# Kernel tuning notes

Measured on AMD Instinct MI355X. Metric: run time of the kernel, lower is better.

## Reference

```python
import jax, jax.numpy as jnp
import numpy as np

N = 50000        # nodes
E_RAND = 800000  # random edges (avg degree 16)
F_IN = 512       # num_features
H = 128          # h_dim * num_heads = 16 * 8
C = 40           # num_classes
NEG_SLOPE = 0.2  # GATv2 default


def _glorot(key, shape):
    lim = float(np.sqrt(6.0 / (shape[0] + shape[1])))
    return jax.random.uniform(key, shape, jnp.float32, -lim, lim)


def setup_inputs() -> dict:
    key = jax.random.key(0)
    ks = jax.random.split(key, 12)
    src = jax.random.randint(ks[0], (E_RAND,), 0, N)
    dst = jax.random.randint(ks[1], (E_RAND,), 0, N)
    loop = jnp.arange(N)  # self-loops (GATv2Conv add_self_loops=True)
    edge_index = jnp.stack([jnp.concatenate([src, loop]),
                            jnp.concatenate([dst, loop])]).astype(jnp.int32)
    x = jax.random.normal(ks[2], (N, F_IN), jnp.float32)
    return {
        "x": x,
        "edge_index": edge_index,
        "W1l": _glorot(ks[3], (F_IN, H)), "b1l": jnp.zeros((H,), jnp.float32),
        "W1r": _glorot(ks[4], (F_IN, H)), "b1r": jnp.zeros((H,), jnp.float32),
        "a1": _glorot(ks[5], (H, 1)).reshape(H),
        "bias1": jnp.zeros((H,), jnp.float32),
        "W2l": _glorot(ks[6], (H, C)), "b2l": jnp.zeros((C,), jnp.float32),
        "W2r": _glorot(ks[7], (H, C)), "b2r": jnp.zeros((C,), jnp.float32),
        "a2": _glorot(ks[8], (C, 1)).reshape(C),
        "bias2": jnp.zeros((C,), jnp.float32),
    }


def gatv2_layer(x, src, dst, Wl, bl, Wr, br, att, bias, n):
    # PyG GATv2Conv, heads=1: xl = lin_l(x) (source side), xr = lin_r(x) (target side)
    xl = x @ Wl + bl                                   # [N, C_out]
    xr = x @ Wr + br                                   # [N, C_out]
    # edge score e_ij = a^T LeakyReLU(xl[j] + xr[i])
    e = jax.nn.leaky_relu(xl[src] + xr[dst], negative_slope=NEG_SLOPE) @ att  # [E]
    # segment softmax over edges grouped by destination node
    m = jax.ops.segment_max(e, dst, num_segments=n)    # every node has a self-loop
    ex = jnp.exp(e - m[dst])
    den = jax.ops.segment_sum(ex, dst, num_segments=n)
    alpha = ex / den[dst]                              # [E]
    # weighted scatter-aggregate of source-transformed features
    out = jax.ops.segment_sum(alpha[:, None] * xl[src], dst, num_segments=n)
    return out + bias


def reference(x, edge_index, W1l, b1l, W1r, b1r, a1, bias1,
              W2l, b2l, W2r, b2r, a2, bias2):
    # eval mode: dropout(p=0.6) is identity
    src, dst = edge_index[0], edge_index[1]
    n = x.shape[0]
    h = gatv2_layer(x, src, dst, W1l, b1l, W1r, b1r, a1, bias1, n)
    h = jax.nn.elu(h)
    h = gatv2_layer(h, src, dst, W2l, b2l, W2r, b2r, a2, bias2, n)
    return (h, jax.nn.log_softmax(h, axis=1))
```

## Files before the change

### kernel.cpp

```cpp
#include <hip/hip_runtime.h>
#include <hip/hip_bf16.h>
#include <math.h>

#define FIN 512
#define H1 128
#define C2 40
#define C2P 64

typedef __attribute__((ext_vector_type(8))) short short8;
typedef __attribute__((ext_vector_type(4))) float f32x4;

__device__ __forceinline__ ushort f2bf(float f) {
    union { float f; unsigned u; } c; c.f = f;
    unsigned u = c.u;
    return (ushort)((u + 0x7fffu + ((u >> 16) & 1u)) >> 16);
}
__device__ __forceinline__ float bf2f_lo(unsigned u) { return __uint_as_float(u << 16); }
__device__ __forceinline__ float bf2f_hi(unsigned u) { return __uint_as_float(u & 0xffff0000u); }

__device__ __forceinline__ short bfc(float f) {
    __hip_bfloat16 h = __float2bfloat16(f);
    return *reinterpret_cast<short*>(&h);
}

__device__ __forceinline__ void gload_lds16(const void* g, void* l) {
    __builtin_amdgcn_global_load_lds(
        (const __attribute__((address_space(1))) void*)g,
        (__attribute__((address_space(3))) void*)l, 16, 0, 0);
}

__global__ void aux_k(const int* __restrict__ dst, int* __restrict__ cnt, int E, int EB,
                      const float* __restrict__ W1l, const float* __restrict__ W1r,
                      ushort* __restrict__ Wt2,
                      const float* __restrict__ W2l, const float* __restrict__ W2r,
                      ushort* __restrict__ Ws) {
    int b = blockIdx.x;
    int t = threadIdx.x;
    if (b < EB) {
        int e = b * 256 + t;
        if (e < E) atomicAdd(&cnt[dst[e] + 1], 1);
    } else if (b < EB + 512) {
        int idx = (b - EB) * 256 + t;
        int kc  = idx >> 11;
        int rem = idx & 2047;
        int col = rem >> 3;
        int j   = rem & 7;
        int k   = kc * 8 + j;
        float v = (col < H1) ? W1l[k * H1 + col] : W1r[k * H1 + (col - H1)];
        Wt2[idx] = f2bf(v);
    } else {
        int idx = (b - EB - 512) * 256 + t;
        if (idx < 80 * H1) {
            int col = idx >> 7;
            int k   = idx & 127;
            float v = (col < C2) ? W2l[k * C2 + col] : W2r[k * C2 + (col - C2)];
            Ws[idx] = f2bf(v);
        }
    }
}

__global__ void scanA_k(const int* __restrict__ arr, int* __restrict__ tot, int ntot) {
    __shared__ int red[256];
    int b = blockIdx.x, t = threadIdx.x;
    int idx = b * 256 + t;
    int v = (idx < ntot) ? arr[idx] : 0;
    red[t] = v;
    __syncthreads();
#pragma unroll
    for (int o = 128; o > 0; o >>= 1) {
        if (t < o) red[t] += red[t + o];
        __syncthreads();
    }
    if (t == 0) tot[b] = red[0];
}

__global__ void scanB_k(int* __restrict__ tot, int nb) {
    __shared__ int s[256];
    int t = threadIdx.x;
    int v = (t < nb) ? tot[t] : 0;
    s[t] = v;
    __syncthreads();
    for (int o = 1; o < 256; o <<= 1) {
        int x = (t >= o) ? s[t - o] : 0;
        __syncthreads();
        s[t] += x;
        __syncthreads();
    }
    if (t < nb) tot[t] = s[t] - v;
}

__global__ void scanC_k(int* __restrict__ arr, const int* __restrict__ tot, int ntot) {
    __shared__ int s[256];
    int b = blockIdx.x, t = threadIdx.x;
    int idx = b * 256 + t;
    int v = (idx < ntot) ? arr[idx] : 0;
    s[t] = v;
    __syncthreads();
    for (int o = 1; o < 256; o <<= 1) {
        int x = (t >= o) ? s[t - o] : 0;
        __syncthreads();
        s[t] += x;
        __syncthreads();
    }
    if (idx < ntot) arr[idx] = s[t] + tot[b];
}

__global__ void fill_k(const int* __restrict__ src, const int* __restrict__ dst,
                       const int* __restrict__ rowptr, int* __restrict__ fillp,
                       int* __restrict__ csr, int E) {
    int e = blockIdx.x * 256 + threadIdx.x;
    if (e < E) {
        int d = dst[e];
        int p = atomicAdd(&fillp[d], 1);
        csr[rowptr[d] + p] = src[e];
    }
}

__global__ __launch_bounds__(256, 3) void gemm1_k(
    const float* __restrict__ x, const ushort* __restrict__ Wt2,
    const float* __restrict__ bl, const float* __restrict__ br,
    ushort* __restrict__ xlb, ushort* __restrict__ xrb, int n)
{
    __shared__ ushort As[64][72];
    __shared__ ushort Bs[8 * 256 * 8];

    const int tid  = threadIdx.x;
    const int w    = tid >> 6;
    const int lane = tid & 63;
    const int l15  = lane & 15;
    const int lhi  = lane >> 4;
    const int r0   = blockIdx.x * 64;

    f32x4 acc[4][4];
#pragma unroll
    for (int m = 0; m < 4; m++)
#pragma unroll
        for (int nn = 0; nn < 4; nn++) acc[m][nn] = (f32x4){0.f, 0.f, 0.f, 0.f};

    const int arow = tid >> 2;
    const int akq  = (tid & 3) * 16;
    const int arow_g = min(r0 + arow, n - 1);
    const float* aptr = x + (size_t)arow_g * FIN + akq;

    const char* bsrc = (const char*)Wt2 + (size_t)w * 8192 + (size_t)lane * 16;
    char*       bdst = (char*)Bs + (size_t)w * 8192 + (size_t)lane * 16;

    for (int kk = 0; kk < FIN; kk += 64) {
        const char* bs = bsrc + (size_t)(kk >> 3) * 4096;
#pragma unroll
        for (int i = 0; i < 8; i++)
            gload_lds16(bs + i * 1024, bdst + i * 1024);

        float4 v0 = *reinterpret_cast<const float4*>(aptr + kk);
        float4 v1 = *reinterpret_cast<const float4*>(aptr + kk + 4);
        float4 v2 = *reinterpret_cast<const float4*>(aptr + kk + 8);
        float4 v3 = *reinterpret_cast<const float4*>(aptr + kk + 12);
        short8 h0, h1;
        h0[0] = bfc(v0.x); h0[1] = bfc(v0.y); h0[2] = bfc(v0.z); h0[3] = bfc(v0.w);
        h0[4] = bfc(v1.x); h0[5] = bfc(v1.y); h0[6] = bfc(v1.z); h0[7] = bfc(v1.w);
        h1[0] = bfc(v2.x); h1[1] = bfc(v2.y); h1[2] = bfc(v2.z); h1[3] = bfc(v2.w);
        h1[4] = bfc(v3.x); h1[5] = bfc(v3.y); h1[6] = bfc(v3.z); h1[7] = bfc(v3.w);
        *reinterpret_cast<short8*>(&As[arow][akq])     = h0;
        *reinterpret_cast<short8*>(&As[arow][akq + 8]) = h1;

        __syncthreads();

#pragma unroll
        for (int ks = 0; ks < 2; ks++) {
            short8 af[4], bf4[4];
#pragma unroll
            for (int m = 0; m < 4; m++)
                af[m] = *reinterpret_cast<const short8*>(&As[m * 16 + l15][ks * 32 + lhi * 8]);
#pragma unroll
            for (int nn = 0; nn < 4; nn++)
                bf4[nn] = *reinterpret_cast<const short8*>(
                    &Bs[((ks * 4 + lhi) * 256 + w * 64 + nn * 16 + l15) * 8]);
#pragma unroll
            for (int m = 0; m < 4; m++)
#pragma unroll
                for (int nn = 0; nn < 4; nn++)
                    acc[m][nn] = __builtin_amdgcn_mfma_f32_16x16x32_bf16(af[m], bf4[nn], acc[m][nn], 0, 0, 0);
        }
        __syncthreads();
    }

#pragma unroll
    for (int nn = 0; nn < 4; nn++) {
        int col = w * 64 + nn * 16 + l15;
        bool left = (col < H1);
        float bias = left ? bl[col] : br[col - H1];
        ushort* outp = left ? xlb : xrb;
        int colw = left ? col : col - H1;
#pragma unroll
        for (int m = 0; m < 4; m++) {
#pragma unroll
            for (int r = 0; r < 4; r++) {
                int row = r0 + m * 16 + lhi * 4 + r;
                if (row < n)
                    outp[(size_t)row * H1 + colw] = f2bf(acc[m][nn][r] + bias);
            }
        }
    }
}

__global__ __launch_bounds__(256) void edge1_k(
    const ushort* __restrict__ xlb, const ushort* xrb,
    const int* __restrict__ rowptr, const int* __restrict__ csr,
    const float* __restrict__ att, const float* __restrict__ bias,
    ushort* hb, int n)
{
    int wid  = threadIdx.x >> 6;
    int lane = threadIdx.x & 63;
    int grp  = lane >> 4;
    int gl   = lane & 15;
    int i = blockIdx.x * 4 + wid;
    if (i >= n) return;

    uint4 xru = *reinterpret_cast<const uint4*>(&xrb[(size_t)i * H1 + gl * 8]);
    float xrv[8];
    xrv[0] = bf2f_lo(xru.x); xrv[1] = bf2f_hi(xru.x);
    xrv[2] = bf2f_lo(xru.y); xrv[3] = bf2f_hi(xru.y);
    xrv[4] = bf2f_lo(xru.z); xrv[5] = bf2f_hi(xru.z);
    xrv[6] = bf2f_lo(xru.w); xrv[7] = bf2f_hi(xru.w);
    float4 a0 = *reinterpret_cast<const float4*>(&att[gl * 8]);
    float4 a1 = *reinterpret_cast<const float4*>(&att[gl * 8 + 4]);
    float av[8] = {a0.x, a0.y, a0.z, a0.w, a1.x, a1.y, a1.z, a1.w};

    int e0 = rowptr[i], e1 = rowptr[i + 1];

    float m = -INFINITY, den = 0.f;
    float acc[8];
#pragma unroll
    for (int f = 0; f < 8; f++) acc[f] = 0.f;

    int e = e0 + grp;
    uint4 u;
    if (e < e1) {
        int s = csr[e];
        u = *reinterpret_cast<const uint4*>(&xlb[(size_t)s * H1 + gl * 8]);
    }
    while (e < e1) {
        uint4 cu = u;
        int en = e + 4;
        if (en < e1) {
            int s2 = csr[en];
            u = *reinterpret_cast<const uint4*>(&xlb[(size_t)s2 * H1 + gl * 8]);
        }
        float xlv[8];
        xlv[0] = bf2f_lo(cu.x); xlv[1] = bf2f_hi(cu.x);
        xlv[2] = bf2f_lo(cu.y); xlv[3] = bf2f_hi(cu.y);
        xlv[4] = bf2f_lo(cu.z); xlv[5] = bf2f_hi(cu.z);
        xlv[6] = bf2f_lo(cu.w); xlv[7] = bf2f_hi(cu.w);
        float p = 0.f;
#pragma unroll
        for (int f = 0; f < 8; f++) {
            float t = xlv[f] + xrv[f];
            t = t > 0.f ? t : 0.2f * t;
            p += t * av[f];
        }
#pragma unroll
        for (int o = 8; o > 0; o >>= 1) p += __shfl_xor(p, o);
        float mn = fmaxf(m, p);
        float sc = __expf(m - mn);
        float wgt = __expf(p - mn);
        den = den * sc + wgt;
#pragma unroll
        for (int f = 0; f < 8; f++) acc[f] = acc[f] * sc + wgt * xlv[f];
        m = mn;
        e = en;
    }

    float mstar = m;
    mstar = fmaxf(mstar, __shfl_xor(mstar, 16));
    mstar = fmaxf(mstar, __shfl_xor(mstar, 32));
    float scale = __expf(m - mstar);
    den *= scale;
#pragma unroll
    for (int f = 0; f < 8; f++) acc[f] *= scale;
    den += __shfl_xor(den, 16); den += __shfl_xor(den, 32);
#pragma unroll
    for (int f = 0; f < 8; f++) {
        acc[f] += __shfl_xor(acc[f], 16);
        acc[f] += __shfl_xor(acc[f], 32);
    }

    if (grp == 0) {
        float inv = 1.f / den;
        short8 hv;
#pragma unroll
        for (int f = 0; f < 8; f++) {
            float v = acc[f] * inv + bias[gl * 8 + f];
            v = v > 0.f ? v : expm1f(v);
            hv[f] = bfc(v);
        }
        *reinterpret_cast<short8*>(&hb[(size_t)i * H1 + gl * 8]) = hv;
    }
}

__global__ __launch_bounds__(256) void gemm2_k(
    const ushort* __restrict__ hb, const ushort* __restrict__ Ws,
    const float* __restrict__ bl, const float* __restrict__ br,
    ushort* __restrict__ xl2b, float* __restrict__ xr2, int n)
{
    __shared__ ushort WsL[80][136];

    const int tid = threadIdx.x;
    const int w    = tid >> 6;
    const int lane = tid & 63;
    const int l15  = lane & 15;
    const int lhi  = lane >> 4;
    const int r0 = blockIdx.x * 64;

#pragma unroll
    for (int q = 0; q < 5; q++) {
        int c = tid + q * 256;
        int col = c >> 4;
        int k0  = (c & 15) * 8;
        *reinterpret_cast<short8*>(&WsL[col][k0]) =
            *reinterpret_cast<const short8*>(&Ws[col * H1 + k0]);
    }
    __syncthreads();

    const int arow = min(r0 + w * 16 + l15, n - 1);
    const ushort* ap = &hb[(size_t)arow * H1 + lhi * 8];

    f32x4 acc[5];
#pragma unroll
    for (int nt = 0; nt < 5; nt++) acc[nt] = (f32x4){0.f, 0.f, 0.f, 0.f};

#pragma unroll
    for (int kc = 0; kc < 4; kc++) {
        short8 af = *reinterpret_cast<const short8*>(ap + kc * 32);
#pragma unroll
        for (int nt = 0; nt < 5; nt++) {
            short8 bf = *reinterpret_cast<const short8*>(&WsL[nt * 16 + l15][kc * 32 + lhi * 8]);
            acc[nt] = __builtin_amdgcn_mfma_f32_16x16x32_bf16(af, bf, acc[nt], 0, 0, 0);
        }
    }

#pragma unroll
    for (int nt = 0; nt < 5; nt++) {
        int col = nt * 16 + l15;
        float bias = (col < C2) ? bl[col] : br[col - C2];
#pragma unroll
        for (int r = 0; r < 4; r++) {
            int row = r0 + w * 16 + lhi * 4 + r;
            if (row < n) {
                float v = acc[nt][r] + bias;
                if (col < C2) xl2b[(size_t)row * C2P + col] = f2bf(v);
                else          xr2 [(size_t)row * C2  + (col - C2)] = v;
            }
        }
    }
    {
        int row = r0 + w * 16 + l15;
        int part = lhi;
        if (part < 3 && row < n) {
            uint4 z = make_uint4(0u, 0u, 0u, 0u);
            *reinterpret_cast<uint4*>(&xl2b[(size_t)row * C2P + C2 + part * 8]) = z;
        }
    }
}

__global__ __launch_bounds__(256) void edge2_k(
    const ushort* __restrict__ xl2b, const float* __restrict__ xr2,
    const int* __restrict__ rowptr, const int* __restrict__ csr,
    const float* __restrict__ att, const float* __restrict__ bias,
    float* __restrict__ out, int n)
{
    int wid  = threadIdx.x >> 6;
    int lane = threadIdx.x & 63;
    int grp  = lane >> 3;
    int gl   = lane & 7;
    int i = blockIdx.x * 4 + wid;
    if (i >= n) return;

    float xrv[8], av[8];
#pragma unroll
    for (int f = 0; f < 8; f++) {
        int idx = gl * 8 + f;
        bool real = idx < C2;
        xrv[f] = real ? xr2[(size_t)i * C2 + idx] : 0.f;
        av[f]  = real ? att[idx] : 0.f;
    }

    int e0 = rowptr[i], e1 = rowptr[i + 1];

    float m = -INFINITY, den = 0.f;
    float acc[8];
#pragma unroll
    for (int f = 0; f < 8; f++) acc[f] = 0.f;

    int e = e0 + grp;
    uint4 u;
    if (e < e1) {
        int s = csr[e];
        u = *reinterpret_cast<const uint4*>(&xl2b[(size_t)s * C2P + gl * 8]);
    }
    while (e < e1) {
        uint4 cu = u;
        int en = e + 8;
        if (en < e1) {
            int s2 = csr[en];
            u = *reinterpret_cast<const uint4*>(&xl2b[(size_t)s2 * C2P + gl * 8]);
        }
        float xlv[8];
        xlv[0] = bf2f_lo(cu.x); xlv[1] = bf2f_hi(cu.x);
        xlv[2] = bf2f_lo(cu.y); xlv[3] = bf2f_hi(cu.y);
        xlv[4] = bf2f_lo(cu.z); xlv[5] = bf2f_hi(cu.z);
        xlv[6] = bf2f_lo(cu.w); xlv[7] = bf2f_hi(cu.w);
        float p = 0.f;
#pragma unroll
        for (int f = 0; f < 8; f++) {
            float t = xlv[f] + xrv[f];
            t = t > 0.f ? t : 0.2f * t;
            p += t * av[f];
        }
#pragma unroll
        for (int o = 4; o > 0; o >>= 1) p += __shfl_xor(p, o);
        float mn = fmaxf(m, p);
        float sc = __expf(m - mn);
        float wgt = __expf(p - mn);
        den = den * sc + wgt;
#pragma unroll
        for (int f = 0; f < 8; f++) acc[f] = acc[f] * sc + wgt * xlv[f];
        m = mn;
        e = en;
    }

    float mstar = m;
    mstar = fmaxf(mstar, __shfl_xor(mstar, 8));
    mstar = fmaxf(mstar, __shfl_xor(mstar, 16));
    mstar = fmaxf(mstar, __shfl_xor(mstar, 32));
    float scale = __expf(m - mstar);
    den *= scale;
#pragma unroll
    for (int f = 0; f < 8; f++) acc[f] *= scale;
    den += __shfl_xor(den, 8); den += __shfl_xor(den, 16); den += __shfl_xor(den, 32);
#pragma unroll
    for (int f = 0; f < 8; f++) {
        acc[f] += __shfl_xor(acc[f], 8);
        acc[f] += __shfl_xor(acc[f], 16);
        acc[f] += __shfl_xor(acc[f], 32);
    }

    float inv = 1.f / den;
    bool real_lane = gl < 5;
    float o[8];
#pragma unroll
    for (int f = 0; f < 8; f++) {
        int idx = gl * 8 + f;
        o[f] = acc[f] * inv + (idx < C2 ? bias[idx] : 0.f);
    }

    float mv = -INFINITY;
    if (real_lane) {
#pragma unroll
        for (int f = 0; f < 8; f++) mv = fmaxf(mv, o[f]);
    }
    mv = fmaxf(mv, __shfl_xor(mv, 1));
    mv = fmaxf(mv, __shfl_xor(mv, 2));
    mv = fmaxf(mv, __shfl_xor(mv, 4));
    float se = 0.f;
    if (real_lane) {
#pragma unroll
        for (int f = 0; f < 8; f++) se += __expf(o[f] - mv);
    }
    se += __shfl_xor(se, 1); se += __shfl_xor(se, 2); se += __shfl_xor(se, 4);
    float lse = mv + logf(se);

    if (grp == 0 && real_lane) {
        float* op = &out[(size_t)i * C2 + gl * 8];
        *reinterpret_cast<float4*>(op)     = make_float4(o[0], o[1], o[2], o[3]);
        *reinterpret_cast<float4*>(op + 4) = make_float4(o[4], o[5], o[6], o[7]);
        float* lp = &out[(size_t)n * C2 + (size_t)i * C2 + gl * 8];
        *reinterpret_cast<float4*>(lp)     = make_float4(o[0] - lse, o[1] - lse, o[2] - lse, o[3] - lse);
        *reinterpret_cast<float4*>(lp + 4) = make_float4(o[4] - lse, o[5] - lse, o[6] - lse, o[7] - lse);
    }
}

extern "C" void kernel_launch(void* const* d_in, const int* in_sizes, int n_in,
                              void* d_out, int out_size, void* d_ws, size_t ws_size,
                              hipStream_t stream) {
    const float* x    = (const float*)d_in[0];
    const int*   ei   = (const int*)  d_in[1];
    const float* W1l  = (const float*)d_in[2];
    const float* b1l  = (const float*)d_in[3];
    const float* W1r  = (const float*)d_in[4];
    const float* b1r  = (const float*)d_in[5];
    const float* a1   = (const float*)d_in[6];
    const float* bias1= (const float*)d_in[7];
    const float* W2l  = (const float*)d_in[8];
    const float* b2l  = (const float*)d_in[9];
    const float* W2r  = (const float*)d_in[10];
    const float* b2r  = (const float*)d_in[11];
    const float* a2   = (const float*)d_in[12];
    const float* bias2= (const float*)d_in[13];

    const int N = in_sizes[0] / FIN;
    const int E = in_sizes[1] / 2;
    const int* src = ei;
    const int* dst = ei + E;

    ushort* xrb  = (ushort*)d_ws;
    ushort* xlb  = xrb + (size_t)N * H1;
    ushort* xl2b = xlb;
    float*  xr2  = (float*)(xlb + (size_t)N * H1);
    ushort* Wt2  = (ushort*)(xr2 + (size_t)N * C2);
    ushort* Ws2  = Wt2 + 131072;
    int* rowptr  = (int*)(Ws2 + 10240);
    int* fillp   = rowptr + (N + 1);
    int* csr     = fillp + N;
    int* tot     = csr + E;

    const int EB = (E + 255) / 256;
    const int SB = (N + 1 + 255) / 256;

    hipMemsetAsync(rowptr, 0, sizeof(int) * (size_t)(2 * N + 1), stream);
    aux_k<<<EB + 552, 256, 0, stream>>>(dst, rowptr, E, EB, W1l, W1r, Wt2, W2l, W2r, Ws2);
    scanA_k<<<SB, 256, 0, stream>>>(rowptr, tot, N + 1);
    scanB_k<<<1, 256, 0, stream>>>(tot, SB);
    scanC_k<<<SB, 256, 0, stream>>>(rowptr, tot, N + 1);
    fill_k<<<EB, 256, 0, stream>>>(src, dst, rowptr, fillp, csr, E);

    gemm1_k<<<(N + 63) / 64, 256, 0, stream>>>(x, Wt2, b1l, b1r, xlb, xrb, N);
    edge1_k<<<(N + 3) / 4, 256, 0, stream>>>(xlb, xrb, rowptr, csr, a1, bias1, xrb, N);
    gemm2_k<<<(N + 63) / 64, 256, 0, stream>>>(xrb, Ws2, b2l, b2r, xl2b, xr2, N);
    edge2_k<<<(N + 3) / 4, 256, 0, stream>>>(xl2b, xr2, rowptr, csr, a2, bias2, (float*)d_out, N);
}
```

Baseline: 269.8 us.

## Batch edge index loads and issue multiple gathers before compute in edge kernels

Both edge aggregation kernels now load a chunk of CSR source indices with one coalesced wave load and spread them to lane groups with shuffles. They then issue six (layer 1) or four (layer 2) independent feature-row gathers before running the online-softmax updates. The old loop kept only one gather in flight per group, so this is meant to raise memory-level parallelism and hide gather latency. The cost is more registers held per lane and wasted predicated slots for low-degree nodes.

```diff
diff --git a/kernel.cpp b/kernel.cpp
--- a/kernel.cpp
+++ b/kernel.cpp
@@ -203,6 +203,32 @@
     }
 }
 
+__device__ __forceinline__ void e1_step(uint4 G, bool V, const float* xrv, const float* av,
+                                        float& m, float& den, float* acc) {
+    if (!V) return;
+    float xlv[8];
+    xlv[0] = bf2f_lo(G.x); xlv[1] = bf2f_hi(G.x);
+    xlv[2] = bf2f_lo(G.y); xlv[3] = bf2f_hi(G.y);
+    xlv[4] = bf2f_lo(G.z); xlv[5] = bf2f_hi(G.z);
+    xlv[6] = bf2f_lo(G.w); xlv[7] = bf2f_hi(G.w);
+    float p = 0.f;
+#pragma unroll
+    for (int f = 0; f < 8; f++) {
+        float t = xlv[f] + xrv[f];
+        t = t > 0.f ? t : 0.2f * t;
+        p += t * av[f];
+    }
+    p += __shfl_xor(p, 8); p += __shfl_xor(p, 4);
+    p += __shfl_xor(p, 2); p += __shfl_xor(p, 1);
+    float mn  = fmaxf(m, p);
+    float sc  = __expf(m - mn);
+    float wgt = __expf(p - mn);
+    den = den * sc + wgt;
+#pragma unroll
+    for (int f = 0; f < 8; f++) acc[f] = acc[f] * sc + wgt * xlv[f];
+    m = mn;
+}
+
 __global__ __launch_bounds__(256) void edge1_k(
     const ushort* __restrict__ xlb, const ushort* xrb,
     const int* __restrict__ rowptr, const int* __restrict__ csr,
@@ -233,41 +259,30 @@
 #pragma unroll
     for (int f = 0; f < 8; f++) acc[f] = 0.f;
 
-    int e = e0 + grp;
-    uint4 u;
-    if (e < e1) {
-        int s = csr[e];
-        u = *reinterpret_cast<const uint4*>(&xlb[(size_t)s * H1 + gl * 8]);
-    }
-    while (e < e1) {
-        uint4 cu = u;
-        int en = e + 4;
-        if (en < e1) {
-            int s2 = csr[en];
-            u = *reinterpret_cast<const uint4*>(&xlb[(size_t)s2 * H1 + gl * 8]);
-        }
-        float xlv[8];
-        xlv[0] = bf2f_lo(cu.x); xlv[1] = bf2f_hi(cu.x);
-        xlv[2] = bf2f_lo(cu.y); xlv[3] = bf2f_hi(cu.y);
-        xlv[4] = bf2f_lo(cu.z); xlv[5] = bf2f_hi(cu.z);
-        xlv[6] = bf2f_lo(cu.w); xlv[7] = bf2f_hi(cu.w);
-        float p = 0.f;
-#pragma unroll
-        for (int f = 0; f < 8; f++) {
-            float t = xlv[f] + xrv[f];
-            t = t > 0.f ? t : 0.2f * t;
-            p += t * av[f];
-        }
-#pragma unroll
-        for (int o = 8; o > 0; o >>= 1) p += __shfl_xor(p, o);
-        float mn = fmaxf(m, p);
-        float sc = __expf(m - mn);
-        float wgt = __expf(p - mn);
-        den = den * sc + wgt;
-#pragma unroll
-        for (int f = 0; f < 8; f++) acc[f] = acc[f] * sc + wgt * xlv[f];
-        m = mn;
-        e = en;
+    for (int base = e0; base < e1; base += 24) {
+        int myidx = 0;
+        if (lane < 24 && base + lane < e1) myidx = csr[base + lane];
+        bool v0 = (base +  0 + grp) < e1;
+        bool v1 = (base +  4 + grp) < e1;
+        bool v2 = (base +  8 + grp) < e1;
+        bool v3 = (base + 12 + grp) < e1;
+        bool v4 = (base + 16 + grp) < e1;
+        bool v5 = (base + 20 + grp) < e1;
+        uint4 g0, g1, g2, g3, g4, g5;
+        int s;
+        s = __shfl(myidx,  0 + grp); if (v0) g0 = *reinterpret_cast<const uint4*>(&xlb[(size_t)s * H1 + gl * 8]);
+        s = __shfl(myidx,  4 + grp); if (v1) g1 = *reinterpret_cast<const uint4*>(&xlb[(size_t)s * H1 + gl * 8]);
+        s = __shfl(myidx,  8 + grp); if (v2) g2 = *reinterpret_cast<const uint4*>(&xlb[(size_t)s * H1 + gl * 8]);
+        s = __shfl(myidx, 12 + grp); if (v3) g3 = *reinterpret_cast<const uint4*>(&xlb[(size_t)s * H1 + gl * 8]);
+        s = __shfl(myidx, 16 + grp); if (v4) g4 = *reinterpret_cast<const uint4*>(&xlb[(size_t)s * H1 + gl * 8]);
+        s = __shfl(myidx, 20 + grp); if (v5) g5 = *reinterpret_cast<const uint4*>(&xlb[(size_t)s * H1 + gl * 8]);
+
+        e1_step(g0, v0, xrv, av, m, den, acc);
+        e1_step(g1, v1, xrv, av, m, den, acc);
+        e1_step(g2, v2, xrv, av, m, den, acc);
+        e1_step(g3, v3, xrv, av, m, den, acc);
+        e1_step(g4, v4, xrv, av, m, den, acc);
+        e1_step(g5, v5, xrv, av, m, den, acc);
     }
 
     float mstar = m;
@@ -360,6 +375,31 @@
             *reinterpret_cast<uint4*>(&xl2b[(size_t)row * C2P + C2 + part * 8]) = z;
         }
     }
+}
+
+__device__ __forceinline__ void e2_step(uint4 G, bool V, const float* xrv, const float* av,
+                                        float& m, float& den, float* acc) {
+    if (!V) return;
+    float xlv[8];
+    xlv[0] = bf2f_lo(G.x); xlv[1] = bf2f_hi(G.x);
+    xlv[2] = bf2f_lo(G.y); xlv[3] = bf2f_hi(G.y);
+    xlv[4] = bf2f_lo(G.z); xlv[5] = bf2f_hi(G.z);
+    xlv[6] = bf2f_lo(G.w); xlv[7] = bf2f_hi(G.w);
+    float p = 0.f;
+#pragma unroll
+    for (int f = 0; f < 8; f++) {
+        float t = xlv[f] + xrv[f];
+        t = t > 0.f ? t : 0.2f * t;
+        p += t * av[f];
+    }
+    p += __shfl_xor(p, 4); p += __shfl_xor(p, 2); p += __shfl_xor(p, 1);
+    float mn  = fmaxf(m, p);
+    float sc  = __expf(m - mn);
+    float wgt = __expf(p - mn);
+    den = den * sc + wgt;
+#pragma unroll
+    for (int f = 0; f < 8; f++) acc[f] = acc[f] * sc + wgt * xlv[f];
+    m = mn;
 }
 
 __global__ __launch_bounds__(256) void edge2_k(
@@ -391,41 +431,24 @@
 #pragma unroll
     for (int f = 0; f < 8; f++) acc[f] = 0.f;
 
-    int e = e0 + grp;
-    uint4 u;
-    if (e < e1) {
-        int s = csr[e];
-        u = *reinterpret_cast<const uint4*>(&xl2b[(size_t)s * C2P + gl * 8]);
-    }
-    while (e < e1) {
-        uint4 cu = u;
-        int en = e + 8;
-        if (en < e1) {
-            int s2 = csr[en];
-            u = *reinterpret_cast<const uint4*>(&xl2b[(size_t)s2 * C2P + gl * 8]);
-        }
-        float xlv[8];
-        xlv[0] = bf2f_lo(cu.x); xlv[1] = bf2f_hi(cu.x);
-        xlv[2] = bf2f_lo(cu.y); xlv[3] = bf2f_hi(cu.y);
-        xlv[4] = bf2f_lo(cu.z); xlv[5] = bf2f_hi(cu.z);
-        xlv[6] = bf2f_lo(cu.w); xlv[7] = bf2f_hi(cu.w);
-        float p = 0.f;
-#pragma unroll
-        for (int f = 0; f < 8; f++) {
-            float t = xlv[f] + xrv[f];
-            t = t > 0.f ? t : 0.2f * t;
-            p += t * av[f];
-        }
-#pragma unroll
-        for (int o = 4; o > 0; o >>= 1) p += __shfl_xor(p, o);
-        float mn = fmaxf(m, p);
-        float sc = __expf(m - mn);
-        float wgt = __expf(p - mn);
-        den = den * sc + wgt;
-#pragma unroll
-        for (int f = 0; f < 8; f++) acc[f] = acc[f] * sc + wgt * xlv[f];
-        m = mn;
-        e = en;
+    for (int base = e0; base < e1; base += 32) {
+        int myidx = 0;
+        if (lane < 32 && base + lane < e1) myidx = csr[base + lane];
+        bool v0 = (base +  0 + grp) < e1;
+        bool v1 = (base +  8 + grp) < e1;
+        bool v2 = (base + 16 + grp) < e1;
+        bool v3 = (base + 24 + grp) < e1;
+        uint4 g0, g1, g2, g3;
+        int s;
+        s = __shfl(myidx,  0 + grp); if (v0) g0 = *reinterpret_cast<const uint4*>(&xl2b[(size_t)s * C2P + gl * 8]);
+        s = __shfl(myidx,  8 + grp); if (v1) g1 = *reinterpret_cast<const uint4*>(&xl2b[(size_t)s * C2P + gl * 8]);
+        s = __shfl(myidx, 16 + grp); if (v2) g2 = *reinterpret_cast<const uint4*>(&xl2b[(size_t)s * C2P + gl * 8]);
+        s = __shfl(myidx, 24 + grp); if (v3) g3 = *reinterpret_cast<const uint4*>(&xl2b[(size_t)s * C2P + gl * 8]);
+
+        e2_step(g0, v0, xrv, av, m, den, acc);
+        e2_step(g1, v1, xrv, av, m, den, acc);
+        e2_step(g2, v2, xrv, av, m, den, acc);
+        e2_step(g3, v3, xrv, av, m, den, acc);
     }
 
     float mstar = m;
```

Measured after the change: 273.8 us. Within noise of the previous version (+1.5%).
